# Performance work log

Hardware: AMD Instinct MI355X
Metric: run time of the kernel (lower is better)

## Reference

```python
import jax, jax.numpy as jnp
import numpy as np

B, T, C = 2, 2048, 1024
NH = 16
HS = C // NH


def setup_inputs() -> dict:
    key = jax.random.key(0)
    k1, k2, k3 = jax.random.split(key, 3)
    scale = 1.0 / np.sqrt(C)
    return {
        "x": jax.random.normal(k1, (B, T, C), dtype=jnp.float32),
        "W_attn": jax.random.normal(k2, (C, 3 * C), dtype=jnp.float32) * scale,
        "b_attn": jnp.zeros((3 * C,), dtype=jnp.float32),
        "W_proj": jax.random.normal(k3, (C, C), dtype=jnp.float32) * scale,
        "b_proj": jnp.zeros((C,), dtype=jnp.float32),
    }


def reference(x, W_attn, b_attn, W_proj, b_proj) -> jnp.ndarray:
    Bx, Tx, Cx = x.shape
    qkv = x @ W_attn + b_attn                      # [B, T, 3C]
    q, k, v = jnp.split(qkv, 3, axis=-1)           # each [B, T, C]

    def heads(t):  # [B, T, C] -> [B, NH, T, HS]
        return t.reshape(Bx, Tx, NH, HS).transpose(0, 2, 1, 3)

    q, k, v = heads(q), heads(k), heads(v)
    att = jnp.einsum("bhqd,bhkd->bhqk", q, k) / jnp.sqrt(jnp.float32(HS))
    causal = jnp.tril(jnp.ones((Tx, Tx), dtype=bool))
    att = jnp.where(causal, att, -jnp.inf)
    att = jax.nn.softmax(att, axis=-1)
    y = jnp.einsum("bhqk,bhkd->bhqd", att, v)      # [B, NH, T, HS]
    y = y.transpose(0, 2, 1, 3).reshape(Bx, Tx, Cx)
    return y @ W_proj + b_proj
```

## Files before the change

kernel.cpp:

```cpp
#include <hip/hip_runtime.h>
#include <hip/hip_bf16.h>
#include <stdint.h>

#define DEV static __device__ __forceinline__

typedef __attribute__((ext_vector_type(8))) __bf16 bf16x8;
typedef __attribute__((ext_vector_type(4))) __bf16 bf16x4;
typedef __attribute__((ext_vector_type(4))) float f32x4;
typedef __attribute__((ext_vector_type(16))) float f32x16;

#define BB 2
#define TT 2048
#define CC 1024
#define NHH 16
#define HSS 64
#define BT 4096
#define N3 3072

DEV unsigned short f2bf(float f) {
  union { float f; uint32_t u; } v; v.f = f;
  uint32_t r = v.u + 0x7FFFu + ((v.u >> 16) & 1u);
  return (unsigned short)(r >> 16);
}

typedef const __attribute__((address_space(1))) unsigned int* gas_t;
typedef __attribute__((address_space(3))) unsigned int* las_t;

DEV void glds16(const void* g, void* l) {
  __builtin_amdgcn_global_load_lds((gas_t)g, (las_t)l, 16, 0, 0);
}

DEV f32x4 mfma16(bf16x8 a, bf16x8 b, f32x4 c) {
  return __builtin_amdgcn_mfma_f32_16x16x32_bf16(a, b, c, 0, 0, 0);
}
DEV f32x16 mfma32(bf16x8 a, bf16x8 b, f32x16 c) {
  return __builtin_amdgcn_mfma_f32_32x32x16_bf16(a, b, c, 0, 0, 0);
}

DEV bf16x8 ld8(const unsigned short* p) { return *(const bf16x8*)p; }

DEV f32x16 z16() {
  f32x16 v;
#pragma unroll
  for (int i = 0; i < 16; i++) v[i] = 0.f;
  return v;
}

__global__ void k_conv(const float* __restrict__ in, unsigned short* __restrict__ out, int n4) {
  int i = blockIdx.x * blockDim.x + threadIdx.x;
  int stride = gridDim.x * blockDim.x;
  for (; i < n4; i += stride) {
    float4 v = ((const float4*)in)[i];
    ushort4 o;
    o.x = f2bf(v.x); o.y = f2bf(v.y); o.z = f2bf(v.z); o.w = f2bf(v.w);
    ((ushort4*)out)[i] = o;
  }
}

__global__ void k_transp(const float* __restrict__ in, unsigned short* __restrict__ out,
                         int K, int N) {
  __shared__ float tile[32][33];
  int n0 = blockIdx.x * 32, k0 = blockIdx.y * 32;
  int tx = threadIdx.x, ty = threadIdx.y;
  for (int r = ty; r < 32; r += 8)
    tile[r][tx] = in[(size_t)(k0 + r) * N + n0 + tx];
  __syncthreads();
  for (int r = ty; r < 32; r += 8)
    out[(size_t)(n0 + r) * K + k0 + tx] = f2bf(tile[tx][r]);
}

template <int OUT_BF16>
__global__ __launch_bounds__(256) void k_gemm(const unsigned short* __restrict__ A,
                                              const unsigned short* __restrict__ Bt,
                                              const float* __restrict__ bias,
                                              void* __restrict__ Cout,
                                              int N, int K, int gx) {
  __shared__ __align__(16) unsigned short As[2][128 * 32];
  __shared__ __align__(16) unsigned short Bs[2][128 * 32];
  const int t = threadIdx.x;
  const int wave = t >> 6, l = t & 63, lr = l & 15, lg = l >> 4;
  const int cpx = gridDim.x >> 3;
  const int sw = ((int)blockIdx.x & 7) * cpx + ((int)blockIdx.x >> 3);
  const int m0 = (sw / gx) * 128, n0 = (sw % gx) * 128;
  const int wm = wave >> 1, wn = wave & 1;

  f32x4 acc[4][4] = {};

  const unsigned short* gA = A + (size_t)(m0 + (t >> 2)) * K + (t & 3) * 8;
  const unsigned short* gB = Bt + (size_t)(n0 + (t >> 2)) * K + (t & 3) * 8;
  const size_t rstep = (size_t)64 * K;

#define GSTAGE(buf_, k_)                                                  \
  do {                                                                    \
    glds16(gA + (k_), (char*)As[buf_] + wave * 1024);                     \
    glds16(gA + rstep + (k_), (char*)As[buf_] + 4096 + wave * 1024);      \
    glds16(gB + (k_), (char*)Bs[buf_] + wave * 1024);                     \
    glds16(gB + rstep + (k_), (char*)Bs[buf_] + 4096 + wave * 1024);      \
  } while (0)

  GSTAGE(0, 0);
  asm volatile("s_waitcnt vmcnt(0)" ::: "memory");
  __builtin_amdgcn_s_barrier();
  __builtin_amdgcn_sched_barrier(0);

  int cur = 0;
  for (int k0 = 0; k0 < K; k0 += 32) {
    if (k0 + 32 < K) GSTAGE(cur ^ 1, k0 + 32);
    __builtin_amdgcn_sched_barrier(0);
    bf16x8 av[4], bv[4];
#pragma unroll
    for (int i = 0; i < 4; i++) {
      av[i] = ld8(As[cur] + (wm * 64 + i * 16 + lr) * 32 + lg * 8);
      bv[i] = ld8(Bs[cur] + (wn * 64 + i * 16 + lr) * 32 + lg * 8);
    }
#pragma unroll
    for (int i = 0; i < 4; i++)
#pragma unroll
      for (int j = 0; j < 4; j++)
        acc[i][j] = mfma16(av[i], bv[j], acc[i][j]);
    if (k0 + 32 < K) asm volatile("s_waitcnt vmcnt(0)" ::: "memory");
    __builtin_amdgcn_s_barrier();
    __builtin_amdgcn_sched_barrier(0);
    cur ^= 1;
  }
#undef GSTAGE

#pragma unroll
  for (int j2 = 0; j2 < 4; j2++) {
    int col = n0 + wn * 64 + j2 * 16 + lr;
    float bv_ = bias[col];
#pragma unroll
    for (int i = 0; i < 4; i++) {
      int row = m0 + wm * 64 + i * 16 + lg * 4;
#pragma unroll
      for (int r = 0; r < 4; r++) {
        float v = acc[i][j2][r] + bv_;
        if (OUT_BF16)
          ((unsigned short*)Cout)[(size_t)(row + r) * N + col] = f2bf(v);
        else
          ((float*)Cout)[(size_t)(row + r) * N + col] = v;
      }
    }
  }
}

__global__ void k_vt(const unsigned short* __restrict__ qkv, unsigned short* __restrict__ vt) {
  __shared__ unsigned short tile[64][65];
  int bh = blockIdx.y, t0 = blockIdx.x * 64;
  int b = bh >> 4, h = bh & 15;
  int tx = threadIdx.x, ty = threadIdx.y;
  const unsigned short* src = qkv + (size_t)(b * TT + t0) * N3 + 2 * CC + h * HSS;
  for (int r = ty; r < 64; r += 4)
    tile[r][tx] = src[(size_t)r * N3 + tx];
  __syncthreads();
  unsigned short* dst = vt + (size_t)bh * HSS * TT + t0;
  for (int r = ty; r < 64; r += 4)
    dst[(size_t)r * TT + tx] = tile[tx][r];
}

__global__ __launch_bounds__(512) void k_attn(const unsigned short* __restrict__ qkv,
                                              const unsigned short* __restrict__ vt,
                                              unsigned short* __restrict__ y) {
  __shared__ __align__(16) unsigned short Ks[3][128 * 64];
  __shared__ __align__(16) unsigned short Vs[3][128 * 64];
  __shared__ __align__(16) unsigned short Ps[8][32 * 64];
  __shared__ float Msh[4][64];
  __shared__ float Lsh[4][64];
  const int t = threadIdx.x;
  const int w = t >> 6, l = t & 63, lq = l & 31, hl = l >> 5;
  const int qsub = w & 3, par = w >> 2;
  const int id = blockIdx.x;
  const int bh = (id & 7) + 8 * ((id >> 3) & 3);
  const int p = id >> 5;
  const int b = bh >> 4, head = bh & 15;
  const int jA = 15 - p, jB = p;
  const int mA = jA + 1;
  const int NT = 17;
  const float cexp = 0.18033688011112042f;
  const float THR = 40.0f;

#define SWZ(r_) ((((r_) & 7) ^ (((r_) >> 3) & 3)) << 4)

  const int myswz = SWZ(lq);
  int offs[4];
#pragma unroll
  for (int s = 0; s < 4; s++) offs[s] = (32 * s + 16 * hl) ^ myswz;

  const int off0 = w * 1024 + l * 16;
  const int off1 = 8192 + w * 1024 + l * 16;
  const int rk0 = off0 >> 7, rk1 = off1 >> 7;
  const int ck0 = (off0 & 127) ^ SWZ(rk0), ck1 = (off1 & 127) ^ SWZ(rk1);
  const int rv0 = rk0 & 63, rv1 = rk1 & 63;
  const int cv0 = (off0 & 127) ^ SWZ(rv0), cv1 = (off1 & 127) ^ SWZ(rv1);
  const char* gK0 = (const char*)(qkv + (size_t)(b * TT + rk0) * N3 + CC + head * HSS) + ck0;
  const char* gK1 = (const char*)(qkv + (size_t)(b * TT + rk1) * N3 + CC + head * HSS) + ck1;
  const char* gV0 = (const char*)(vt + ((size_t)bh * HSS + rv0) * TT) + cv0;
  const char* gV1 = (const char*)(vt + ((size_t)bh * HSS + rv1) * TT + 64) + cv1;
  const int dK0 = w * 1024, dK1 = 8192 + w * 1024;

#define STAGE(slot_, kvt_)                                                \
  do {                                                                    \
    size_t kb = (size_t)(kvt_) * (128 * N3 * 2);                          \
    size_t vb = (size_t)(kvt_) * 256;                                     \
    glds16(gK0 + kb, (char*)Ks[slot_] + dK0);                             \
    glds16(gK1 + kb, (char*)Ks[slot_] + dK1);                             \
    glds16(gV0 + vb, (char*)Vs[slot_] + dK0);                             \
    glds16(gV1 + vb, (char*)Vs[slot_] + dK1);                             \
  } while (0)

#define WRITE_OUT()                                                       \
  do {                                                                    \
    float l_q = l_ln + __shfl_xor(l_ln, 32);                              \
    float inv = 1.0f / l_q;                                               \
    unsigned short* ybase = y + (size_t)(b * TT + q0w + lq) * CC + head * HSS; \
    _Pragma("unroll")                                                     \
    for (int g = 0; g < 4; g++) {                                         \
      ushort4 wv;                                                         \
      wv.x = f2bf(oa[4 * g + 0] * inv); wv.y = f2bf(oa[4 * g + 1] * inv); \
      wv.z = f2bf(oa[4 * g + 2] * inv); wv.w = f2bf(oa[4 * g + 3] * inv); \
      *(ushort4*)(ybase + 8 * g + 4 * hl) = wv;                           \
      ushort4 wv2;                                                        \
      wv2.x = f2bf(ob[4 * g + 0] * inv); wv2.y = f2bf(ob[4 * g + 1] * inv); \
      wv2.z = f2bf(ob[4 * g + 2] * inv); wv2.w = f2bf(ob[4 * g + 3] * inv); \
      *(ushort4*)(ybase + 32 + 8 * g + 4 * hl) = wv2;                     \
    }                                                                     \
  } while (0)

#define MERGE()                                                           \
  do {                                                                    \
    __builtin_amdgcn_s_barrier();                                         \
    if (par) {                                                            \
      float* poa = (float*)Ps[w];                                         \
      float* pob = (float*)Ps[w - 4];                                     \
      _Pragma("unroll")                                                   \
      for (int g = 0; g < 16; g++) { poa[g * 64 + l] = oa[g]; pob[g * 64 + l] = ob[g]; } \
      Msh[qsub][l] = m_s; Lsh[qsub][l] = l_ln;                            \
    }                                                                     \
    asm volatile("s_waitcnt lgkmcnt(0)" ::: "memory");                    \
    __builtin_amdgcn_s_barrier();                                         \
    __builtin_amdgcn_sched_barrier(0);                                    \
    if (!par) {                                                           \
      float m1 = Msh[qsub][l], l1 = Lsh[qsub][l];                         \
      float mstar = fmaxf(m_s, m1);                                       \
      float a0 = __builtin_amdgcn_exp2f((m_s - mstar) * cexp);            \
      float a1 = __builtin_amdgcn_exp2f((m1 - mstar) * cexp);             \
      const float* poa = (const float*)Ps[w + 4];                         \
      const float* pob = (const float*)Ps[w];                             \
      _Pragma("unroll")                                                   \
      for (int g = 0; g < 16; g++) {                                      \
        oa[g] = oa[g] * a0 + poa[g * 64 + l] * a1;                        \
        ob[g] = ob[g] * a0 + pob[g * 64 + l] * a1;                        \
      }                                                                   \
      l_ln = l_ln * a0 + l1 * a1;                                         \
      WRITE_OUT();                                                        \
    }                                                                     \
    __builtin_amdgcn_s_barrier();                                         \
  } while (0)

  int q0w = jA * 128 + qsub * 32;
  const unsigned short* qp = qkv + (size_t)(b * TT + q0w + lq) * N3 + head * HSS + hl * 8;
  bf16x8 qf0 = ld8(qp), qf1 = ld8(qp + 16), qf2 = ld8(qp + 32), qf3 = ld8(qp + 48);
  float m_s = -INFINITY, l_ln = 0.f;
  f32x16 oa = z16(), ob = z16();
  char* prow = (char*)Ps[w] + lq * 128;

  STAGE(0, 0);
  int cur = 0;

  for (int seq = 0; seq < NT; ++seq) {
    if (seq == mA) {
      MERGE();
      q0w = jB * 128 + qsub * 32;
      const unsigned short* qp2 = qkv + (size_t)(b * TT + q0w + lq) * N3 + head * HSS + hl * 8;
      qf0 = ld8(qp2); qf1 = ld8(qp2 + 16); qf2 = ld8(qp2 + 32); qf3 = ld8(qp2 + 48);
      m_s = -INFINITY; l_ln = 0.f;
      oa = z16(); ob = z16();
    }

    const int kvt = (seq < mA) ? seq : (seq - mA);
    if (seq + 1 < NT) {
      int s2 = seq + 1;
      int kvt2 = (s2 < mA) ? s2 : (s2 - mA);
      int nxt = (cur == 2) ? 0 : cur + 1;
      STAGE(nxt, kvt2);
      __builtin_amdgcn_sched_barrier(0);
      asm volatile("s_waitcnt vmcnt(4)" ::: "memory");
    } else {
      asm volatile("s_waitcnt vmcnt(0)" ::: "memory");
    }
    __builtin_amdgcn_s_barrier();
    __builtin_amdgcn_sched_barrier(0);

    const int mybuf = cur;
    cur = (cur == 2) ? 0 : cur + 1;

    const int kv0w = kvt * 128 + 64 * par;
    if (kv0w > q0w + 31) continue;

    const unsigned short* Kb = Ks[mybuf];
    const unsigned short* Vb = Vs[mybuf];

    const char* krA = (const char*)Kb + (64 * par + lq) * 128;
    const char* krB = krA + 32 * 128;
    f32x16 sa = z16(), sb = z16();
    __builtin_amdgcn_s_setprio(1);
    {
      bf16x8 ka, kb8;
      ka = ld8((const unsigned short*)(krA + offs[0]));
      kb8 = ld8((const unsigned short*)(krB + offs[0]));
      sa = mfma32(ka, qf0, sa); sb = mfma32(kb8, qf0, sb);
      ka = ld8((const unsigned short*)(krA + offs[1]));
      kb8 = ld8((const unsigned short*)(krB + offs[1]));
      sa = mfma32(ka, qf1, sa); sb = mfma32(kb8, qf1, sb);
      ka = ld8((const unsigned short*)(krA + offs[2]));
      kb8 = ld8((const unsigned short*)(krB + offs[2]));
      sa = mfma32(ka, qf2, sa); sb = mfma32(kb8, qf2, sb);
      ka = ld8((const unsigned short*)(krA + offs[3]));
      kb8 = ld8((const unsigned short*)(krB + offs[3]));
      sa = mfma32(ka, qf3, sa); sb = mfma32(kb8, qf3, sb);
    }
    __builtin_amdgcn_s_setprio(0);

    if (kv0w + 63 > q0w) {
      const int q = q0w + lq;
#pragma unroll
      for (int g = 0; g < 16; g++) {
        int kvl = kv0w + (g & 3) + 8 * (g >> 2) + 4 * hl;
        if (kvl > q) sa[g] = -INFINITY;
        if (kvl + 32 > q) sb[g] = -INFINITY;
      }
    }

    float tmax = -INFINITY;
#pragma unroll
    for (int g = 0; g < 16; g++) tmax = fmaxf(tmax, fmaxf(sa[g], sb[g]));
    tmax = fmaxf(tmax, __shfl_xor(tmax, 32));

    if (!__all(tmax <= m_s + THR)) {
      float m_new = fmaxf(m_s, tmax);
      float alpha = __builtin_amdgcn_exp2f((m_s - m_new) * cexp);
      l_ln *= alpha;
#pragma unroll
      for (int g = 0; g < 16; g++) { oa[g] *= alpha; ob[g] *= alpha; }
      m_s = m_new;
    }

    const float mc = m_s * cexp;
    float tsum = 0.f;
#pragma unroll
    for (int g = 0; g < 16; g++) {
      sa[g] = __builtin_amdgcn_exp2f(__builtin_fmaf(sa[g], cexp, -mc));
      sb[g] = __builtin_amdgcn_exp2f(__builtin_fmaf(sb[g], cexp, -mc));
      tsum += sa[g] + sb[g];
    }
    l_ln += tsum;

#pragma unroll
    for (int u2 = 0; u2 < 4; u2++) {
      bf16x4 w0, w1;
#pragma unroll
      for (int r = 0; r < 4; r++) { w0[r] = (__bf16)sa[4 * u2 + r]; w1[r] = (__bf16)sb[4 * u2 + r]; }
      *(bf16x4*)(prow + ((16 * u2 + 8 * hl) ^ myswz)) = w0;
      *(bf16x4*)(prow + ((64 + 16 * u2 + 8 * hl) ^ myswz)) = w1;
    }
    asm volatile("s_waitcnt lgkmcnt(0)" ::: "memory");
    __builtin_amdgcn_sched_barrier(0);
    bf16x8 pf0 = ld8((const unsigned short*)(prow + offs[0]));
    bf16x8 pf1 = ld8((const unsigned short*)(prow + offs[1]));
    bf16x8 pf2 = ld8((const unsigned short*)(prow + offs[2]));
    bf16x8 pf3 = ld8((const unsigned short*)(prow + offs[3]));

    const char* vrA = (const char*)Vb + par * 8192 + lq * 128;
    const char* vrB = vrA + 32 * 128;
    __builtin_amdgcn_s_setprio(1);
    {
      bf16x8 va, vb8;
      va = ld8((const unsigned short*)(vrA + offs[0]));
      vb8 = ld8((const unsigned short*)(vrB + offs[0]));
      oa = mfma32(va, pf0, oa); ob = mfma32(vb8, pf0, ob);
      va = ld8((const unsigned short*)(vrA + offs[1]));
      vb8 = ld8((const unsigned short*)(vrB + offs[1]));
      oa = mfma32(va, pf1, oa); ob = mfma32(vb8, pf1, ob);
      va = ld8((const unsigned short*)(vrA + offs[2]));
      vb8 = ld8((const unsigned short*)(vrB + offs[2]));
      oa = mfma32(va, pf2, oa); ob = mfma32(vb8, pf2, ob);
      va = ld8((const unsigned short*)(vrA + offs[3]));
      vb8 = ld8((const unsigned short*)(vrB + offs[3]));
      oa = mfma32(va, pf3, oa); ob = mfma32(vb8, pf3, ob);
    }
    __builtin_amdgcn_s_setprio(0);
  }

  MERGE();
#undef STAGE
#undef WRITE_OUT
#undef MERGE
#undef SWZ
}

extern "C" void kernel_launch(void* const* d_in, const int* in_sizes, int n_in,
                              void* d_out, int out_size, void* d_ws, size_t ws_size,
                              hipStream_t stream) {
  const float* x = (const float*)d_in[0];
  const float* W_attn = (const float*)d_in[1];
  const float* b_attn = (const float*)d_in[2];
  const float* W_proj = (const float*)d_in[3];
  const float* b_proj = (const float*)d_in[4];

  char* ws = (char*)d_ws;
  unsigned short* xb   = (unsigned short*)(ws);
  unsigned short* wabt = (unsigned short*)(ws + 8388608);
  unsigned short* wpbt = (unsigned short*)(ws + 14680064);
  unsigned short* qkvb = (unsigned short*)(ws + 16777216);
  unsigned short* vt   = (unsigned short*)(ws + 41943040);
  unsigned short* yb   = (unsigned short*)(ws + 50331648);

  k_conv<<<2048, 256, 0, stream>>>(x, xb, BT * CC / 4);
  k_transp<<<dim3(N3 / 32, CC / 32), dim3(32, 8), 0, stream>>>(W_attn, wabt, CC, N3);
  k_transp<<<dim3(CC / 32, CC / 32), dim3(32, 8), 0, stream>>>(W_proj, wpbt, CC, CC);
  k_gemm<1><<<dim3(768), 256, 0, stream>>>(xb, wabt, b_attn, qkvb, N3, CC, 24);
  k_vt<<<dim3(TT / 64, BB * NHH), dim3(64, 4), 0, stream>>>(qkvb, vt);
  k_attn<<<dim3(256), 512, 0, stream>>>(qkvb, vt, yb);
  k_gemm<0><<<dim3(256), 256, 0, stream>>>(yb, wpbt, b_proj, d_out, CC, CC, 8);
}
```

Baseline: 116.1 us.

## Split attention blocks into 256-thread halves with double-buffered KV and pooled merge

The attention kernel goes from 256 blocks of 512 threads to 512 blocks of 256 threads, each handling half of a 128-row query tile (64 rows). KV staging drops from triple to double buffering, with a full wait and barrier before each prefetch. The V tile layout changes to 64x128. The merge scratch reuses the idle K/V buffer instead of dedicated Ps/Msh/Lsh arrays. Shared memory per block shrinks, so more blocks can be resident, but each block reloads the same K/V tiles and there is less load/compute overlap.

```diff
diff --git a/kernel.cpp b/kernel.cpp
--- a/kernel.cpp
+++ b/kernel.cpp
@@ -158,24 +158,24 @@
     dst[(size_t)r * TT + tx] = tile[tx][r];
 }
 
-__global__ __launch_bounds__(512) void k_attn(const unsigned short* __restrict__ qkv,
+__global__ __launch_bounds__(256) void k_attn(const unsigned short* __restrict__ qkv,
                                               const unsigned short* __restrict__ vt,
                                               unsigned short* __restrict__ y) {
-  __shared__ __align__(16) unsigned short Ks[3][128 * 64];
-  __shared__ __align__(16) unsigned short Vs[3][128 * 64];
-  __shared__ __align__(16) unsigned short Ps[8][32 * 64];
-  __shared__ float Msh[4][64];
-  __shared__ float Lsh[4][64];
+  __shared__ __align__(16) unsigned short Ks[2][128 * 64];
+  __shared__ __align__(16) unsigned short Vs[2][64 * 128];
+  __shared__ __align__(16) unsigned short Ps[4][32 * 64];
   const int t = threadIdx.x;
   const int w = t >> 6, l = t & 63, lq = l & 31, hl = l >> 5;
-  const int qsub = w & 3, par = w >> 2;
+  const int qsub = w & 1, par = w >> 1;
   const int id = blockIdx.x;
   const int bh = (id & 7) + 8 * ((id >> 3) & 3);
-  const int p = id >> 5;
+  const int uu = id >> 5;
+  const int pp = uu & 7, qh = uu >> 3;
   const int b = bh >> 4, head = bh & 15;
-  const int jA = 15 - p, jB = p;
+  const int jA = 15 - pp, jB = pp;
   const int mA = jA + 1;
   const int NT = 17;
+  const int fsA = 1 - (pp & 1);
   const float cexp = 0.18033688011112042f;
   const float THR = 40.0f;
 
@@ -186,26 +186,34 @@
 #pragma unroll
   for (int s = 0; s < 4; s++) offs[s] = (32 * s + 16 * hl) ^ myswz;
 
-  const int off0 = w * 1024 + l * 16;
-  const int off1 = 8192 + w * 1024 + l * 16;
-  const int rk0 = off0 >> 7, rk1 = off1 >> 7;
-  const int ck0 = (off0 & 127) ^ SWZ(rk0), ck1 = (off1 & 127) ^ SWZ(rk1);
-  const int rv0 = rk0 & 63, rv1 = rk1 & 63;
-  const int cv0 = (off0 & 127) ^ SWZ(rv0), cv1 = (off1 & 127) ^ SWZ(rv1);
-  const char* gK0 = (const char*)(qkv + (size_t)(b * TT + rk0) * N3 + CC + head * HSS) + ck0;
-  const char* gK1 = (const char*)(qkv + (size_t)(b * TT + rk1) * N3 + CC + head * HSS) + ck1;
-  const char* gV0 = (const char*)(vt + ((size_t)bh * HSS + rv0) * TT) + cv0;
-  const char* gV1 = (const char*)(vt + ((size_t)bh * HSS + rv1) * TT + 64) + cv1;
-  const int dK0 = w * 1024, dK1 = 8192 + w * 1024;
+  const int u8 = t >> 3;
+  const int ck = ((t & 7) * 16) ^ SWZ(u8);
+  const char* gK = (const char*)(qkv + (size_t)(b * TT + u8) * N3 + CC + head * HSS) + ck;
+  const int v16 = t >> 4;
+  const int ph = (t >> 3) & 1;
+  const int sbyte = (t & 7) * 16;
+  const char* gV[4];
+#pragma unroll
+  for (int i = 0; i < 4; i++) {
+    int row = i * 16 + v16;
+    gV[i] = (const char*)vt + ((size_t)bh * HSS + row) * TT * 2 + ph * 128 +
+            (sbyte ^ SWZ(row));
+  }
 
 #define STAGE(slot_, kvt_)                                                \
   do {                                                                    \
     size_t kb = (size_t)(kvt_) * (128 * N3 * 2);                          \
     size_t vb = (size_t)(kvt_) * 256;                                     \
-    glds16(gK0 + kb, (char*)Ks[slot_] + dK0);                             \
-    glds16(gK1 + kb, (char*)Ks[slot_] + dK1);                             \
-    glds16(gV0 + vb, (char*)Vs[slot_] + dK0);                             \
-    glds16(gV1 + vb, (char*)Vs[slot_] + dK1);                             \
+    char* kd = (char*)Ks[slot_] + t * 16;                                 \
+    char* vd = (char*)Vs[slot_] + t * 16;                                 \
+    glds16(gK + kb, kd);                                                  \
+    glds16(gK + kb + (size_t)32 * N3 * 2, kd + 4096);                     \
+    glds16(gK + kb + (size_t)64 * N3 * 2, kd + 8192);                     \
+    glds16(gK + kb + (size_t)96 * N3 * 2, kd + 12288);                    \
+    glds16(gV[0] + vb, vd);                                               \
+    glds16(gV[1] + vb, vd + 4096);                                        \
+    glds16(gV[2] + vb, vd + 8192);                                        \
+    glds16(gV[3] + vb, vd + 12288);                                       \
   } while (0)
 
 #define WRITE_OUT()                                                       \
@@ -226,26 +234,29 @@
     }                                                                     \
   } while (0)
 
-#define MERGE()                                                           \
+#define MERGE(fs_)                                                        \
   do {                                                                    \
     __builtin_amdgcn_s_barrier();                                         \
+    float* poolK = (float*)(Ks[fs_]);                                     \
+    float* poolV = (float*)(Vs[fs_]);                                     \
     if (par) {                                                            \
-      float* poa = (float*)Ps[w];                                         \
-      float* pob = (float*)Ps[w - 4];                                     \
+      float* poa = poolK + qsub * 1024;                                   \
+      float* pob = poolK + 2048 + qsub * 1024;                            \
       _Pragma("unroll")                                                   \
       for (int g = 0; g < 16; g++) { poa[g * 64 + l] = oa[g]; pob[g * 64 + l] = ob[g]; } \
-      Msh[qsub][l] = m_s; Lsh[qsub][l] = l_ln;                            \
+      poolV[qsub * 64 + l] = m_s;                                         \
+      poolV[128 + qsub * 64 + l] = l_ln;                                  \
     }                                                                     \
     asm volatile("s_waitcnt lgkmcnt(0)" ::: "memory");                    \
     __builtin_amdgcn_s_barrier();                                         \
     __builtin_amdgcn_sched_barrier(0);                                    \
     if (!par) {                                                           \
-      float m1 = Msh[qsub][l], l1 = Lsh[qsub][l];                         \
+      float m1 = poolV[qsub * 64 + l], l1 = poolV[128 + qsub * 64 + l];   \
       float mstar = fmaxf(m_s, m1);                                       \
       float a0 = __builtin_amdgcn_exp2f((m_s - mstar) * cexp);            \
       float a1 = __builtin_amdgcn_exp2f((m1 - mstar) * cexp);             \
-      const float* poa = (const float*)Ps[w + 4];                         \
-      const float* pob = (const float*)Ps[w];                             \
+      const float* poa = poolK + qsub * 1024;                             \
+      const float* pob = poolK + 2048 + qsub * 1024;                      \
       _Pragma("unroll")                                                   \
       for (int g = 0; g < 16; g++) {                                      \
         oa[g] = oa[g] * a0 + poa[g * 64 + l] * a1;                        \
@@ -257,7 +268,7 @@
     __builtin_amdgcn_s_barrier();                                         \
   } while (0)
 
-  int q0w = jA * 128 + qsub * 32;
+  int q0w = jA * 128 + qh * 64 + qsub * 32;
   const unsigned short* qp = qkv + (size_t)(b * TT + q0w + lq) * N3 + head * HSS + hl * 8;
   bf16x8 qf0 = ld8(qp), qf1 = ld8(qp + 16), qf2 = ld8(qp + 32), qf3 = ld8(qp + 48);
   float m_s = -INFINITY, l_ln = 0.f;
@@ -265,40 +276,34 @@
   char* prow = (char*)Ps[w] + lq * 128;
 
   STAGE(0, 0);
-  int cur = 0;
 
   for (int seq = 0; seq < NT; ++seq) {
     if (seq == mA) {
-      MERGE();
-      q0w = jB * 128 + qsub * 32;
+      MERGE(fsA);
+      q0w = jB * 128 + qh * 64 + qsub * 32;
       const unsigned short* qp2 = qkv + (size_t)(b * TT + q0w + lq) * N3 + head * HSS + hl * 8;
       qf0 = ld8(qp2); qf1 = ld8(qp2 + 16); qf2 = ld8(qp2 + 32); qf3 = ld8(qp2 + 48);
       m_s = -INFINITY; l_ln = 0.f;
       oa = z16(); ob = z16();
     }
 
-    const int kvt = (seq < mA) ? seq : (seq - mA);
+    asm volatile("s_waitcnt vmcnt(0)" ::: "memory");
+    __builtin_amdgcn_s_barrier();
+    __builtin_amdgcn_sched_barrier(0);
+
     if (seq + 1 < NT) {
       int s2 = seq + 1;
       int kvt2 = (s2 < mA) ? s2 : (s2 - mA);
-      int nxt = (cur == 2) ? 0 : cur + 1;
-      STAGE(nxt, kvt2);
-      __builtin_amdgcn_sched_barrier(0);
-      asm volatile("s_waitcnt vmcnt(4)" ::: "memory");
-    } else {
-      asm volatile("s_waitcnt vmcnt(0)" ::: "memory");
-    }
-    __builtin_amdgcn_s_barrier();
+      STAGE((s2) & 1, kvt2);
+    }
     __builtin_amdgcn_sched_barrier(0);
 
-    const int mybuf = cur;
-    cur = (cur == 2) ? 0 : cur + 1;
-
+    const int kvt = (seq < mA) ? seq : (seq - mA);
     const int kv0w = kvt * 128 + 64 * par;
     if (kv0w > q0w + 31) continue;
 
-    const unsigned short* Kb = Ks[mybuf];
-    const unsigned short* Vb = Vs[mybuf];
+    const unsigned short* Kb = Ks[seq & 1];
+    const unsigned short* Vb = Vs[seq & 1];
 
     const char* krA = (const char*)Kb + (64 * par + lq) * 128;
     const char* krB = krA + 32 * 128;
@@ -370,8 +375,8 @@
     bf16x8 pf2 = ld8((const unsigned short*)(prow + offs[2]));
     bf16x8 pf3 = ld8((const unsigned short*)(prow + offs[3]));
 
-    const char* vrA = (const char*)Vb + par * 8192 + lq * 128;
-    const char* vrB = vrA + 32 * 128;
+    const char* vrA = (const char*)Vb + lq * 256 + par * 128;
+    const char* vrB = vrA + 32 * 256;
     __builtin_amdgcn_s_setprio(1);
     {
       bf16x8 va, vb8;
@@ -391,7 +396,7 @@
     __builtin_amdgcn_s_setprio(0);
   }
 
-  MERGE();
+  MERGE(1);
 #undef STAGE
 #undef WRITE_OUT
 #undef MERGE
@@ -420,6 +425,6 @@
   k_transp<<<dim3(CC / 32, CC / 32), dim3(32, 8), 0, stream>>>(W_proj, wpbt, CC, CC);
   k_gemm<1><<<dim3(768), 256, 0, stream>>>(xb, wabt, b_attn, qkvb, N3, CC, 24);
   k_vt<<<dim3(TT / 64, BB * NHH), dim3(64, 4), 0, stream>>>(qkvb, vt);
-  k_attn<<<dim3(256), 512, 0, stream>>>(qkvb, vt, yb);
+  k_attn<<<dim3(512), 256, 0, stream>>>(qkvb, vt, yb);
   k_gemm<0><<<dim3(256), 256, 0, stream>>>(yb, wpbt, b_proj, d_out, CC, CC, 8);
 }
```

Measured after the change: 123.3 us. 6.2% more time.

## Deepen GEMM K-tile to 64 with XOR-swizzled LDS layout

Applied to the files above, without the earlier changes.

Doubles the GEMM K-stage from 32 to 64 elements per buffer, halving the number of barrier and wait iterations. It also adds an XOR swizzle to the LDS layout, applied on the global-to-LDS load side and matched on the fragment reads, to avoid bank conflicts with the wider 128-byte rows. The cost is doubled shared memory per block, which may reduce occupancy. The wait-then-barrier is now placed before the prefetch issue.

```diff
diff --git a/kernel.cpp b/kernel.cpp
--- a/kernel.cpp
+++ b/kernel.cpp
@@ -75,8 +75,8 @@
                                               const float* __restrict__ bias,
                                               void* __restrict__ Cout,
                                               int N, int K, int gx) {
-  __shared__ __align__(16) unsigned short As[2][128 * 32];
-  __shared__ __align__(16) unsigned short Bs[2][128 * 32];
+  __shared__ __align__(16) unsigned short As[2][128 * 64];
+  __shared__ __align__(16) unsigned short Bs[2][128 * 64];
   const int t = threadIdx.x;
   const int wave = t >> 6, l = t & 63, lr = l & 15, lg = l >> 4;
   const int cpx = gridDim.x >> 3;
@@ -86,42 +86,60 @@
 
   f32x4 acc[4][4] = {};
 
-  const unsigned short* gA = A + (size_t)(m0 + (t >> 2)) * K + (t & 3) * 8;
-  const unsigned short* gB = Bt + (size_t)(n0 + (t >> 2)) * K + (t & 3) * 8;
-  const size_t rstep = (size_t)64 * K;
-
-#define GSTAGE(buf_, k_)                                                  \
+  int swz[4];
+#pragma unroll
+  for (int i = 0; i < 4; i++)
+    swz[i] = ((lr & 7) ^ ((2 * i + (lr >> 3)) & 3)) << 4;
+
+  const int strow = t >> 3;
+  const int stcol = ((t & 7) * 16) ^ ((((t >> 3) & 7) ^ ((t >> 6) & 3)) << 4);
+  const char* gAc = (const char*)(A + (size_t)(m0 + strow) * K) + stcol;
+  const char* gBc = (const char*)(Bt + (size_t)(n0 + strow) * K) + stcol;
+  const size_t rstep = (size_t)32 * K * 2;
+
+#define GSTAGE(buf_, k0_)                                                 \
   do {                                                                    \
-    glds16(gA + (k_), (char*)As[buf_] + wave * 1024);                     \
-    glds16(gA + rstep + (k_), (char*)As[buf_] + 4096 + wave * 1024);      \
-    glds16(gB + (k_), (char*)Bs[buf_] + wave * 1024);                     \
-    glds16(gB + rstep + (k_), (char*)Bs[buf_] + 4096 + wave * 1024);      \
+    const char* a0 = gAc + (size_t)(k0_) * 2;                             \
+    const char* b0 = gBc + (size_t)(k0_) * 2;                             \
+    char* ad = (char*)As[buf_] + t * 16;                                  \
+    char* bd = (char*)Bs[buf_] + t * 16;                                  \
+    glds16(a0, ad);                                                       \
+    glds16(a0 + rstep, ad + 4096);                                        \
+    glds16(a0 + 2 * rstep, ad + 8192);                                    \
+    glds16(a0 + 3 * rstep, ad + 12288);                                   \
+    glds16(b0, bd);                                                       \
+    glds16(b0 + rstep, bd + 4096);                                        \
+    glds16(b0 + 2 * rstep, bd + 8192);                                    \
+    glds16(b0 + 3 * rstep, bd + 12288);                                   \
   } while (0)
 
+  const int nst = K >> 6;
   GSTAGE(0, 0);
-  asm volatile("s_waitcnt vmcnt(0)" ::: "memory");
-  __builtin_amdgcn_s_barrier();
-  __builtin_amdgcn_sched_barrier(0);
-
-  int cur = 0;
-  for (int k0 = 0; k0 < K; k0 += 32) {
-    if (k0 + 32 < K) GSTAGE(cur ^ 1, k0 + 32);
-    __builtin_amdgcn_sched_barrier(0);
-    bf16x8 av[4], bv[4];
-#pragma unroll
-    for (int i = 0; i < 4; i++) {
-      av[i] = ld8(As[cur] + (wm * 64 + i * 16 + lr) * 32 + lg * 8);
-      bv[i] = ld8(Bs[cur] + (wn * 64 + i * 16 + lr) * 32 + lg * 8);
-    }
-#pragma unroll
-    for (int i = 0; i < 4; i++)
-#pragma unroll
-      for (int j = 0; j < 4; j++)
-        acc[i][j] = mfma16(av[i], bv[j], acc[i][j]);
-    if (k0 + 32 < K) asm volatile("s_waitcnt vmcnt(0)" ::: "memory");
+
+  for (int st = 0; st < nst; ++st) {
+    asm volatile("s_waitcnt vmcnt(0)" ::: "memory");
     __builtin_amdgcn_s_barrier();
     __builtin_amdgcn_sched_barrier(0);
-    cur ^= 1;
+    if (st + 1 < nst) GSTAGE((st + 1) & 1, (st + 1) * 64);
+    __builtin_amdgcn_sched_barrier(0);
+
+    const char* Ab = (const char*)As[st & 1];
+    const char* Bb = (const char*)Bs[st & 1];
+#pragma unroll
+    for (int s = 0; s < 2; s++) {
+      bf16x8 av[4], bv[4];
+#pragma unroll
+      for (int i = 0; i < 4; i++) {
+        int ko = (s * 64 + lg * 16) ^ swz[i];
+        av[i] = ld8((const unsigned short*)(Ab + (wm * 64 + i * 16 + lr) * 128 + ko));
+        bv[i] = ld8((const unsigned short*)(Bb + (wn * 64 + i * 16 + lr) * 128 + ko));
+      }
+#pragma unroll
+      for (int i = 0; i < 4; i++)
+#pragma unroll
+        for (int j = 0; j < 4; j++)
+          acc[i][j] = mfma16(av[i], bv[j], acc[i][j]);
+    }
   }
 #undef GSTAGE
 
```

New measurement: 119.3 us. 2.8% more time.

## Triple-buffer GEMM LDS staging with partial vmcnt waits and MFMA priority

Applied to the files above, without the earlier changes.

Moves the bf16 GEMM's global-to-LDS staging from a double buffer to a triple buffer, prefetching two K-steps ahead. It waits with partial vmcnt counts so loads stay in flight across iterations instead of draining every step. It also raises wave priority around the MFMA block. The cost is more LDS per block, which may lower occupancy, plus an extra barrier per iteration.

```diff
diff --git a/kernel.cpp b/kernel.cpp
--- a/kernel.cpp
+++ b/kernel.cpp
@@ -75,8 +75,8 @@
                                               const float* __restrict__ bias,
                                               void* __restrict__ Cout,
                                               int N, int K, int gx) {
-  __shared__ __align__(16) unsigned short As[2][128 * 32];
-  __shared__ __align__(16) unsigned short Bs[2][128 * 32];
+  __shared__ __align__(16) unsigned short As[3][128 * 32];
+  __shared__ __align__(16) unsigned short Bs[3][128 * 32];
   const int t = threadIdx.x;
   const int wave = t >> 6, l = t & 63, lr = l & 15, lg = l >> 4;
   const int cpx = gridDim.x >> 3;
@@ -92,36 +92,44 @@
 
 #define GSTAGE(buf_, k_)                                                  \
   do {                                                                    \
-    glds16(gA + (k_), (char*)As[buf_] + wave * 1024);                     \
-    glds16(gA + rstep + (k_), (char*)As[buf_] + 4096 + wave * 1024);      \
-    glds16(gB + (k_), (char*)Bs[buf_] + wave * 1024);                     \
-    glds16(gB + rstep + (k_), (char*)Bs[buf_] + 4096 + wave * 1024);      \
+    char* ad = (char*)As[buf_] + t * 16;                                  \
+    char* bd = (char*)Bs[buf_] + t * 16;                                  \
+    glds16(gA + (k_), ad);                                                \
+    glds16(gA + rstep + (k_), ad + 4096);                                 \
+    glds16(gB + (k_), bd);                                                \
+    glds16(gB + rstep + (k_), bd + 4096);                                 \
   } while (0)
 
+  const int nst = K >> 5;
   GSTAGE(0, 0);
-  asm volatile("s_waitcnt vmcnt(0)" ::: "memory");
-  __builtin_amdgcn_s_barrier();
-  __builtin_amdgcn_sched_barrier(0);
-
-  int cur = 0;
-  for (int k0 = 0; k0 < K; k0 += 32) {
-    if (k0 + 32 < K) GSTAGE(cur ^ 1, k0 + 32);
+  GSTAGE(1, 32);
+
+  for (int st = 0; st < nst; ++st) {
+    __builtin_amdgcn_s_barrier();
     __builtin_amdgcn_sched_barrier(0);
+    if (st + 2 < nst) GSTAGE((st + 2) % 3, (st + 2) * 32);
+    __builtin_amdgcn_sched_barrier(0);
+    if (st + 2 < nst)      asm volatile("s_waitcnt vmcnt(8)" ::: "memory");
+    else if (st + 1 < nst) asm volatile("s_waitcnt vmcnt(4)" ::: "memory");
+    else                   asm volatile("s_waitcnt vmcnt(0)" ::: "memory");
+    __builtin_amdgcn_s_barrier();
+    __builtin_amdgcn_sched_barrier(0);
+
+    const unsigned short* Ab = As[st % 3];
+    const unsigned short* Bb = Bs[st % 3];
     bf16x8 av[4], bv[4];
 #pragma unroll
     for (int i = 0; i < 4; i++) {
-      av[i] = ld8(As[cur] + (wm * 64 + i * 16 + lr) * 32 + lg * 8);
-      bv[i] = ld8(Bs[cur] + (wn * 64 + i * 16 + lr) * 32 + lg * 8);
-    }
+      av[i] = ld8(Ab + (wm * 64 + i * 16 + lr) * 32 + lg * 8);
+      bv[i] = ld8(Bb + (wn * 64 + i * 16 + lr) * 32 + lg * 8);
+    }
+    __builtin_amdgcn_s_setprio(1);
 #pragma unroll
     for (int i = 0; i < 4; i++)
 #pragma unroll
       for (int j = 0; j < 4; j++)
         acc[i][j] = mfma16(av[i], bv[j], acc[i][j]);
-    if (k0 + 32 < K) asm volatile("s_waitcnt vmcnt(0)" ::: "memory");
-    __builtin_amdgcn_s_barrier();
-    __builtin_amdgcn_sched_barrier(0);
-    cur ^= 1;
+    __builtin_amdgcn_s_setprio(0);
   }
 #undef GSTAGE
 
```

New measurement: 116.2 us. No clear change (+0.1%).
